# Performance work log

Hardware: AMD Instinct MI355X
Metric: run time of the kernel (lower is better)

## Reference

```python
import jax, jax.numpy as jnp
import numpy as np

B, S, DIN, D = 16, 1024, 64, 64

def setup_inputs() -> dict:
    key = jax.random.key(0)
    kx, kq, kk, kv, kaK, kaV = jax.random.split(key, 6)
    w_scale = 1.0 / np.sqrt(DIN)
    x = jax.random.normal(kx, (B, S, DIN), dtype=jnp.float32)
    Wq = jax.random.normal(kq, (DIN, D), dtype=jnp.float32) * w_scale
    Wk = jax.random.normal(kk, (DIN, D), dtype=jnp.float32) * w_scale
    Wv = jax.random.normal(kv, (DIN, D), dtype=jnp.float32) * w_scale
    # relative-position bias tables alpha_K/alpha_V: [S, S, D]
    alpha_K = jax.random.normal(kaK, (S, S, D), dtype=jnp.float32) * 0.02
    alpha_V = jax.random.normal(kaV, (S, S, D), dtype=jnp.float32) * 0.02
    return {"x": x, "Wq": Wq, "Wk": Wk, "Wv": Wv,
            "alpha_K": alpha_K, "alpha_V": alpha_V}

def reference(x, Wq, Wk, Wv, alpha_K, alpha_V):
    # Relation-aware self-attention (Shaw et al. style), vectorized form of
    # the original per-query loop:
    #   score[b,i,j] = q[b,i] . (k[b,j] + alpha_K[i,j]) / sqrt(D)
    #   z[b,i]       = sum_j softmax_j(score)[b,i,j] * (v[b,j] + alpha_V[i,j])
    d = Wq.shape[1]
    inv_sqrt_d = 1.0 / np.sqrt(d)
    q = jnp.einsum('bsf,fd->bsd', x, Wq)
    k = jnp.einsum('bsf,fd->bsd', x, Wk)
    v = jnp.einsum('bsf,fd->bsd', x, Wv)
    scores = (jnp.einsum('bid,bjd->bij', q, k)
              + jnp.einsum('bid,ijd->bij', q, alpha_K)) * inv_sqrt_d
    attn = jax.nn.softmax(scores, axis=-1)  # [B, S, S]
    z = (jnp.einsum('bij,bjd->bid', attn, v)
         + jnp.einsum('bij,ijd->bid', attn, alpha_V))
    return z, attn
```

## Files before the change

### kernel.cpp

```cpp
#include <hip/hip_runtime.h>
#include <hip/hip_fp16.h>


typedef unsigned short u16;
typedef __attribute__((ext_vector_type(8))) short bhalf8;
typedef __attribute__((ext_vector_type(4))) float fx4;

__device__ __forceinline__ u16 f2bf(float f) {
  union { float f; unsigned u; } v; v.f = f;
  unsigned r = v.u + 0x7FFFu + ((v.u >> 16) & 1u);
  return (u16)(r >> 16);
}

__device__ __forceinline__ bhalf8 pack8(float4 a, float4 b) {
  bhalf8 r;
  r[0] = (short)f2bf(a.x); r[1] = (short)f2bf(a.y); r[2] = (short)f2bf(a.z); r[3] = (short)f2bf(a.w);
  r[4] = (short)f2bf(b.x); r[5] = (short)f2bf(b.y); r[6] = (short)f2bf(b.z); r[7] = (short)f2bf(b.w);
  return r;
}

__global__ __launch_bounds__(256) void k_proj(
    const float* __restrict__ x, const float* __restrict__ Wq,
    const float* __restrict__ Wk, const float* __restrict__ Wv,
    u16* __restrict__ qbf, u16* __restrict__ kbf, float* __restrict__ vf)
{
  __shared__ float wl[3 * 4096];
  const int t = threadIdx.x;
  for (int c = t; c < 4096; c += 256) {
    wl[c] = Wq[c]; wl[4096 + c] = Wk[c]; wl[8192 + c] = Wv[c];
  }
  __syncthreads();
  const int row = blockIdx.x * 64 + (t >> 2);
  const int dbase = (t & 3) * 16;
  float xr[64];
  const float4* xp = (const float4*)(x + (size_t)row * 64);
#pragma unroll
  for (int c = 0; c < 16; ++c) {
    float4 v = xp[c];
    xr[4*c] = v.x; xr[4*c+1] = v.y; xr[4*c+2] = v.z; xr[4*c+3] = v.w;
  }
  float aq[16], ak[16], av[16];
#pragma unroll
  for (int m = 0; m < 16; ++m) { aq[m] = 0.f; ak[m] = 0.f; av[m] = 0.f; }
#pragma unroll
  for (int f = 0; f < 64; ++f) {
    const float xv = xr[f];
    const float* wq = wl + f * 64 + dbase;
#pragma unroll
    for (int m = 0; m < 16; ++m) {
      aq[m] = fmaf(xv, wq[m], aq[m]);
      ak[m] = fmaf(xv, wq[4096 + m], ak[m]);
      av[m] = fmaf(xv, wq[8192 + m], av[m]);
    }
  }
  union { u16 u[16]; uint4 q[2]; } pq, pk;
#pragma unroll
  for (int m = 0; m < 16; ++m) { pq.u[m] = f2bf(aq[m]); pk.u[m] = f2bf(ak[m]); }
  const size_t o = (size_t)row * 64 + dbase;
  *(uint4*)(qbf + o) = pq.q[0]; *(uint4*)(qbf + o + 8) = pq.q[1];
  *(uint4*)(kbf + o) = pk.q[0]; *(uint4*)(kbf + o + 8) = pk.q[1];
  float4* vo = (float4*)(vf + o);
  vo[0] = make_float4(av[0], av[1], av[2], av[3]);
  vo[1] = make_float4(av[4], av[5], av[6], av[7]);
  vo[2] = make_float4(av[8], av[9], av[10], av[11]);
  vo[3] = make_float4(av[12], av[13], av[14], av[15]);
}

__global__ __launch_bounds__(256) void k_qk(
    const u16* __restrict__ qbf, const u16* __restrict__ kbf, __half* __restrict__ qkw)
{
  const int t = threadIdx.x, l = t & 63, w = t >> 6;
  const int b = blockIdx.x & 15, it = blockIdx.x >> 4;
  const int lr = l & 15, lg = l >> 4;
  const int i0 = it * 64 + w * 16;
  const u16* qp = qbf + (size_t)(b * 1024 + i0 + lr) * 64 + lg * 8;
  bhalf8 a0 = *(const bhalf8*)(qp);
  bhalf8 a1 = *(const bhalf8*)(qp + 32);
  for (int jt = 0; jt < 64; ++jt) {
    const int j0 = jt * 16;
    const u16* kp = kbf + (size_t)(b * 1024 + j0 + lr) * 64 + lg * 8;
    bhalf8 b0 = *(const bhalf8*)(kp);
    bhalf8 b1 = *(const bhalf8*)(kp + 32);
    fx4 acc = {0.f, 0.f, 0.f, 0.f};
    acc = __builtin_amdgcn_mfma_f32_16x16x32_bf16(a0, b0, acc, 0, 0, 0);
    acc = __builtin_amdgcn_mfma_f32_16x16x32_bf16(a1, b1, acc, 0, 0, 0);
#pragma unroll
    for (int r = 0; r < 4; ++r) {
      const int i = i0 + lg * 4 + r;
      qkw[((size_t)i * 16 + b) * 1024 + j0 + lr] = __float2half(acc[r]);
    }
  }
}

#define SLD 1028
__global__ __launch_bounds__(256) void k_core(
    const float* __restrict__ aK, const float* __restrict__ aV,
    const u16* __restrict__ qbf, const __half* __restrict__ qkw,
    float* __restrict__ attn_out, float* __restrict__ za)
{
  __shared__ float sl[16 * SLD];
  __shared__ float sinv[16];
  const int i = blockIdx.x;
  const int t = threadIdx.x, l = t & 63, w = t >> 6;
  const int lr = l & 15, lg = l >> 4;

  const __half* qk = qkw + (size_t)i * 16384;
  for (int c = t; c < 16384; c += 256)
    sl[(c >> 10) * SLD + (c & 1023)] = __half2float(qk[c]);

  const u16* qp = qbf + (size_t)(lr * 1024 + i) * 64 + lg * 8;
  bhalf8 a0 = *(const bhalf8*)(qp);
  bhalf8 a1 = *(const bhalf8*)(qp + 32);
  __syncthreads();

  for (int jt = w; jt < 64; jt += 4) {
    const int j0 = jt * 16;
    const float* ap = aK + ((size_t)i * 1024 + j0 + lr) * 64 + lg * 8;
    float4 c0 = *(const float4*)(ap);
    float4 c1 = *(const float4*)(ap + 4);
    float4 c2 = *(const float4*)(ap + 32);
    float4 c3 = *(const float4*)(ap + 36);
    bhalf8 b0 = pack8(c0, c1);
    bhalf8 b1 = pack8(c2, c3);
    fx4 acc = {0.f, 0.f, 0.f, 0.f};
    acc = __builtin_amdgcn_mfma_f32_16x16x32_bf16(a0, b0, acc, 0, 0, 0);
    acc = __builtin_amdgcn_mfma_f32_16x16x32_bf16(a1, b1, acc, 0, 0, 0);
#pragma unroll
    for (int r = 0; r < 4; ++r) {
      const int bb = lg * 4 + r;
      const int j = j0 + lr;
      sl[bb * SLD + j] = (sl[bb * SLD + j] + acc[r]) * 0.125f;
    }
  }
  __syncthreads();

#pragma unroll
  for (int rr = 0; rr < 4; ++rr) {
    const int bb = w * 4 + rr;
    float e[16];
    float m = -3.0e30f;
#pragma unroll
    for (int c = 0; c < 16; ++c) { e[c] = sl[bb * SLD + c * 64 + l]; m = fmaxf(m, e[c]); }
#pragma unroll
    for (int off = 32; off; off >>= 1) m = fmaxf(m, __shfl_xor(m, off));
    float s = 0.f;
#pragma unroll
    for (int c = 0; c < 16; ++c) { e[c] = __expf(e[c] - m); s += e[c]; sl[bb * SLD + c * 64 + l] = e[c]; }
#pragma unroll
    for (int off = 32; off; off >>= 1) s += __shfl_xor(s, off);
    const float inv = 1.0f / s;
    if (l == 0) sinv[bb] = inv;
    float* ao = attn_out + ((size_t)bb * 1024 + i) * 1024;
#pragma unroll
    for (int c = 0; c < 16; ++c) ao[c * 64 + l] = e[c] * inv;
  }
  __syncthreads();

  const int d = l;
  const float* avp = aV + (size_t)i * 65536 + d;
  const float* r0 = sl + (size_t)(w + 0) * SLD;
  const float* r1 = sl + (size_t)(w + 4) * SLD;
  const float* r2 = sl + (size_t)(w + 8) * SLD;
  const float* r3 = sl + (size_t)(w + 12) * SLD;
  float z0 = 0.f, z1 = 0.f, z2 = 0.f, z3 = 0.f;
  for (int j = 0; j < 1024; j += 4) {
    float4 e0 = *(const float4*)(r0 + j);
    float4 e1 = *(const float4*)(r1 + j);
    float4 e2 = *(const float4*)(r2 + j);
    float4 e3 = *(const float4*)(r3 + j);
    float av0 = avp[(size_t)(j + 0) * 64];
    float av1 = avp[(size_t)(j + 1) * 64];
    float av2 = avp[(size_t)(j + 2) * 64];
    float av3 = avp[(size_t)(j + 3) * 64];
    z0 = fmaf(e0.x, av0, z0); z0 = fmaf(e0.y, av1, z0); z0 = fmaf(e0.z, av2, z0); z0 = fmaf(e0.w, av3, z0);
    z1 = fmaf(e1.x, av0, z1); z1 = fmaf(e1.y, av1, z1); z1 = fmaf(e1.z, av2, z1); z1 = fmaf(e1.w, av3, z1);
    z2 = fmaf(e2.x, av0, z2); z2 = fmaf(e2.y, av1, z2); z2 = fmaf(e2.z, av2, z2); z2 = fmaf(e2.w, av3, z2);
    z3 = fmaf(e3.x, av0, z3); z3 = fmaf(e3.y, av1, z3); z3 = fmaf(e3.z, av2, z3); z3 = fmaf(e3.w, av3, z3);
  }
  za[((size_t)i * 16 + w + 0) * 64 + d] = z0 * sinv[w + 0];
  za[((size_t)i * 16 + w + 4) * 64 + d] = z1 * sinv[w + 4];
  za[((size_t)i * 16 + w + 8) * 64 + d] = z2 * sinv[w + 8];
  za[((size_t)i * 16 + w + 12) * 64 + d] = z3 * sinv[w + 12];
}

__global__ __launch_bounds__(256) void k_zv(
    const float* __restrict__ attn, const float* __restrict__ vf,
    const float* __restrict__ za, float* __restrict__ zout)
{
  __shared__ __align__(16) u16 vt[64 * 40];
  const int t = threadIdx.x, l = t & 63, w = t >> 6;
  const int b = blockIdx.x & 15, it = blockIdx.x >> 4;
  const int lr = l & 15, lg = l >> 4;
  const int iw = it * 64 + w * 16;
  fx4 acc[4];
#pragma unroll
  for (int n = 0; n < 4; ++n) acc[n] = (fx4){0.f, 0.f, 0.f, 0.f};
  const int jl = t >> 3;
  const int c0 = (t & 7) * 8;
  for (int ks = 0; ks < 32; ++ks) {
    const int j0 = ks * 32;
    const float* vp = vf + (size_t)(b * 1024 + j0 + jl) * 64 + c0;
    float4 v0 = *(const float4*)(vp);
    float4 v1 = *(const float4*)(vp + 4);
    __syncthreads();
    vt[(c0 + 0) * 40 + jl] = f2bf(v0.x);
    vt[(c0 + 1) * 40 + jl] = f2bf(v0.y);
    vt[(c0 + 2) * 40 + jl] = f2bf(v0.z);
    vt[(c0 + 3) * 40 + jl] = f2bf(v0.w);
    vt[(c0 + 4) * 40 + jl] = f2bf(v1.x);
    vt[(c0 + 5) * 40 + jl] = f2bf(v1.y);
    vt[(c0 + 6) * 40 + jl] = f2bf(v1.z);
    vt[(c0 + 7) * 40 + jl] = f2bf(v1.w);
    __syncthreads();
    const float* apr = attn + (size_t)(b * 1024 + iw + lr) * 1024 + j0 + lg * 8;
    float4 t0 = *(const float4*)(apr);
    float4 t1 = *(const float4*)(apr + 4);
    bhalf8 af = pack8(t0, t1);
#pragma unroll
    for (int n = 0; n < 4; ++n) {
      bhalf8 bf = *(const bhalf8*)(vt + (n * 16 + lr) * 40 + lg * 8);
      acc[n] = __builtin_amdgcn_mfma_f32_16x16x32_bf16(af, bf, acc[n], 0, 0, 0);
    }
  }
#pragma unroll
  for (int n = 0; n < 4; ++n) {
#pragma unroll
    for (int r = 0; r < 4; ++r) {
      const int i = iw + lg * 4 + r;
      const int dd = n * 16 + lr;
      zout[((size_t)b * 1024 + i) * 64 + dd] = acc[n][r] + za[((size_t)i * 16 + b) * 64 + dd];
    }
  }
}

extern "C" void kernel_launch(void* const* d_in, const int* in_sizes, int n_in,
                              void* d_out, int out_size, void* d_ws, size_t ws_size,
                              hipStream_t stream)
{
  const float* x  = (const float*)d_in[0];
  const float* Wq = (const float*)d_in[1];
  const float* Wk = (const float*)d_in[2];
  const float* Wv = (const float*)d_in[3];
  const float* aK = (const float*)d_in[4];
  const float* aV = (const float*)d_in[5];
  float* zout = (float*)d_out;
  float* attn_out = zout + (size_t)16 * 1024 * 64;

  char* ws = (char*)d_ws;
  u16*    qbf = (u16*)(ws);
  u16*    kbf = (u16*)(ws + (size_t)2  * 1024 * 1024);
  float*  vf  = (float*)(ws + (size_t)4  * 1024 * 1024);
  float*  za  = (float*)(ws + (size_t)8  * 1024 * 1024);
  __half* qkw = (__half*)(ws + (size_t)12 * 1024 * 1024);

  hipLaunchKernelGGL(k_proj, dim3(256),  dim3(256), 0, stream, x, Wq, Wk, Wv, qbf, kbf, vf);
  hipLaunchKernelGGL(k_qk,   dim3(256),  dim3(256), 0, stream, qbf, kbf, qkw);
  hipLaunchKernelGGL(k_core, dim3(1024), dim3(256), 0, stream, aK, aV, qbf, qkw, attn_out, za);
  hipLaunchKernelGGL(k_zv,   dim3(256),  dim3(256), 0, stream, attn_out, vf, za, zout);
}
```

Before: 240.7 us.

## Split k_core over two key halves with online softmax to halve LDS

k_core now processes the 1024 keys in two halves of 512, so the shared score buffer shrinks by half and launch bounds request four blocks per CU for higher occupancy. Softmax becomes a two-pass online form: the first half's unnormalised exponentials are written out and rescaled at the end with a correction factor. The alpha_V reduction is also reorganised so each wave covers a key slice for all 16 batches, with a cross-wave sum through shared memory. The hand-written bf16 rounding is replaced by the library __float2bfloat16, and half-precision scores are loaded vectorised. The cost is extra global read-modify-write of attention rows, more barriers, and 16 accumulators per thread.

```diff
diff --git a/kernel.cpp b/kernel.cpp
--- a/kernel.cpp
+++ b/kernel.cpp
@@ -1,21 +1,21 @@
 #include <hip/hip_runtime.h>
 #include <hip/hip_fp16.h>
+#include <hip/hip_bf16.h>
 
 
 typedef unsigned short u16;
 typedef __attribute__((ext_vector_type(8))) short bhalf8;
 typedef __attribute__((ext_vector_type(4))) float fx4;
 
-__device__ __forceinline__ u16 f2bf(float f) {
-  union { float f; unsigned u; } v; v.f = f;
-  unsigned r = v.u + 0x7FFFu + ((v.u >> 16) & 1u);
-  return (u16)(r >> 16);
+__device__ __forceinline__ short b16(float f) {
+  __hip_bfloat16 h = __float2bfloat16(f);
+  return *reinterpret_cast<short*>(&h);
 }
 
 __device__ __forceinline__ bhalf8 pack8(float4 a, float4 b) {
   bhalf8 r;
-  r[0] = (short)f2bf(a.x); r[1] = (short)f2bf(a.y); r[2] = (short)f2bf(a.z); r[3] = (short)f2bf(a.w);
-  r[4] = (short)f2bf(b.x); r[5] = (short)f2bf(b.y); r[6] = (short)f2bf(b.z); r[7] = (short)f2bf(b.w);
+  r[0] = b16(a.x); r[1] = b16(a.y); r[2] = b16(a.z); r[3] = b16(a.w);
+  r[4] = b16(b.x); r[5] = b16(b.y); r[6] = b16(b.z); r[7] = b16(b.w);
   return r;
 }
 
@@ -55,7 +55,7 @@
   }
   union { u16 u[16]; uint4 q[2]; } pq, pk;
 #pragma unroll
-  for (int m = 0; m < 16; ++m) { pq.u[m] = f2bf(aq[m]); pk.u[m] = f2bf(ak[m]); }
+  for (int m = 0; m < 16; ++m) { pq.u[m] = (u16)b16(aq[m]); pk.u[m] = (u16)b16(ak[m]); }
   const size_t o = (size_t)row * 64 + dbase;
   *(uint4*)(qbf + o) = pq.q[0]; *(uint4*)(qbf + o + 8) = pq.q[1];
   *(uint4*)(kbf + o) = pk.q[0]; *(uint4*)(kbf + o + 8) = pk.q[1];
@@ -92,95 +92,151 @@
   }
 }
 
-#define SLD 1028
-__global__ __launch_bounds__(256) void k_core(
+#define SLD2 516
+__global__ __launch_bounds__(256, 4) void k_core(
     const float* __restrict__ aK, const float* __restrict__ aV,
     const u16* __restrict__ qbf, const __half* __restrict__ qkw,
     float* __restrict__ attn_out, float* __restrict__ za)
 {
-  __shared__ float sl[16 * SLD];
-  __shared__ float sinv[16];
+  __shared__ float sl[16 * SLD2];
+  __shared__ float stats[64];
   const int i = blockIdx.x;
   const int t = threadIdx.x, l = t & 63, w = t >> 6;
   const int lr = l & 15, lg = l >> 4;
 
-  const __half* qk = qkw + (size_t)i * 16384;
-  for (int c = t; c < 16384; c += 256)
-    sl[(c >> 10) * SLD + (c & 1023)] = __half2float(qk[c]);
-
   const u16* qp = qbf + (size_t)(lr * 1024 + i) * 64 + lg * 8;
   bhalf8 a0 = *(const bhalf8*)(qp);
   bhalf8 a1 = *(const bhalf8*)(qp + 32);
+
+  float zc[16];
+#pragma unroll
+  for (int b = 0; b < 16; ++b) zc[b] = 0.f;
+
+  for (int h = 0; h < 2; ++h) {
+    const __half* qk = qkw + (size_t)i * 16384 + h * 512;
+    for (int c = t; c < 1024; c += 256) {
+      const int b = c >> 6;
+      const int j8 = (c & 63) * 8;
+      const __half2* hp = (const __half2*)(qk + (size_t)b * 1024 + j8);
+      float2 f0 = __half22float2(hp[0]);
+      float2 f1 = __half22float2(hp[1]);
+      float2 f2 = __half22float2(hp[2]);
+      float2 f3 = __half22float2(hp[3]);
+      float* dst = sl + b * SLD2 + j8;
+      *(float4*)(dst)     = make_float4(f0.x, f0.y, f1.x, f1.y);
+      *(float4*)(dst + 4) = make_float4(f2.x, f2.y, f3.x, f3.y);
+    }
+    __syncthreads();
+
+    for (int tt = 0; tt < 8; ++tt) {
+      const int j0 = (w + tt * 4) * 16;
+      const float* ap = aK + ((size_t)i * 1024 + h * 512 + j0 + lr) * 64 + lg * 8;
+      float4 c0 = *(const float4*)(ap);
+      float4 c1 = *(const float4*)(ap + 4);
+      float4 c2 = *(const float4*)(ap + 32);
+      float4 c3 = *(const float4*)(ap + 36);
+      fx4 acc = {0.f, 0.f, 0.f, 0.f};
+      acc = __builtin_amdgcn_mfma_f32_16x16x32_bf16(a0, pack8(c0, c1), acc, 0, 0, 0);
+      acc = __builtin_amdgcn_mfma_f32_16x16x32_bf16(a1, pack8(c2, c3), acc, 0, 0, 0);
+#pragma unroll
+      for (int r = 0; r < 4; ++r)
+        sl[(lg * 4 + r) * SLD2 + j0 + lr] += acc[r];
+    }
+    __syncthreads();
+
+    if (h == 0) {
+#pragma unroll
+      for (int rr = 0; rr < 4; ++rr) {
+        const int row = w * 4 + rr;
+        float* rp = sl + row * SLD2;
+        float v8[8]; float mx = -3.0e30f;
+#pragma unroll
+        for (int c = 0; c < 8; ++c) { v8[c] = rp[c * 64 + l]; mx = fmaxf(mx, v8[c]); }
+#pragma unroll
+        for (int off = 32; off; off >>= 1) mx = fmaxf(mx, __shfl_xor(mx, off));
+        float sum = 0.f;
+        float* ao = attn_out + ((size_t)row * 1024 + i) * 1024;
+#pragma unroll
+        for (int c = 0; c < 8; ++c) {
+          float e = __expf((v8[c] - mx) * 0.125f);
+          sum += e; rp[c * 64 + l] = e;
+          ao[c * 64 + l] = e;
+        }
+#pragma unroll
+        for (int off = 32; off; off >>= 1) sum += __shfl_xor(sum, off);
+        if (l == 0) { stats[row] = mx; stats[16 + row] = sum; }
+      }
+    } else {
+#pragma unroll
+      for (int rr = 0; rr < 4; ++rr) {
+        const int row = w * 4 + rr;
+        float* rp = sl + row * SLD2;
+        float v8[8]; float mx = -3.0e30f;
+#pragma unroll
+        for (int c = 0; c < 8; ++c) { v8[c] = rp[c * 64 + l]; mx = fmaxf(mx, v8[c]); }
+#pragma unroll
+        for (int off = 32; off; off >>= 1) mx = fmaxf(mx, __shfl_xor(mx, off));
+        const float m1 = stats[row];
+        const float m  = fmaxf(m1, mx);
+        const float corr = __expf((m1 - m) * 0.125f);
+        float e8[8]; float sum = 0.f;
+#pragma unroll
+        for (int c = 0; c < 8; ++c) {
+          e8[c] = __expf((v8[c] - m) * 0.125f);
+          sum += e8[c]; rp[c * 64 + l] = e8[c];
+        }
+#pragma unroll
+        for (int off = 32; off; off >>= 1) sum += __shfl_xor(sum, off);
+        const float inv = 1.0f / (stats[16 + row] * corr + sum);
+        float* ao = attn_out + ((size_t)row * 1024 + i) * 1024 + 512;
+#pragma unroll
+        for (int c = 0; c < 8; ++c) ao[c * 64 + l] = e8[c] * inv;
+        if (l == 0) { stats[32 + row] = corr; stats[48 + row] = inv; }
+      }
+    }
+    __syncthreads();
+
+    if (h == 1) {
+#pragma unroll
+      for (int b = 0; b < 16; ++b) zc[b] *= stats[32 + b];
+    }
+    const float* avp = aV + ((size_t)i * 1024 + h * 512 + w * 128) * 64 + l;
+    for (int jg = 0; jg < 32; ++jg) {
+      const int jl = w * 128 + jg * 4;
+      float a0v = avp[(size_t)(jg * 4 + 0) * 64];
+      float a1v = avp[(size_t)(jg * 4 + 1) * 64];
+      float a2v = avp[(size_t)(jg * 4 + 2) * 64];
+      float a3v = avp[(size_t)(jg * 4 + 3) * 64];
+#pragma unroll
+      for (int b = 0; b < 16; ++b) {
+        float4 e4 = *(const float4*)(sl + b * SLD2 + jl);
+        zc[b] = fmaf(e4.x, a0v, zc[b]);
+        zc[b] = fmaf(e4.y, a1v, zc[b]);
+        zc[b] = fmaf(e4.z, a2v, zc[b]);
+        zc[b] = fmaf(e4.w, a3v, zc[b]);
+      }
+    }
+    __syncthreads();
+  }
+
+#pragma unroll
+  for (int b = 0; b < 16; ++b) sl[(w * 16 + b) * 64 + l] = zc[b];
   __syncthreads();
-
-  for (int jt = w; jt < 64; jt += 4) {
-    const int j0 = jt * 16;
-    const float* ap = aK + ((size_t)i * 1024 + j0 + lr) * 64 + lg * 8;
-    float4 c0 = *(const float4*)(ap);
-    float4 c1 = *(const float4*)(ap + 4);
-    float4 c2 = *(const float4*)(ap + 32);
-    float4 c3 = *(const float4*)(ap + 36);
-    bhalf8 b0 = pack8(c0, c1);
-    bhalf8 b1 = pack8(c2, c3);
-    fx4 acc = {0.f, 0.f, 0.f, 0.f};
-    acc = __builtin_amdgcn_mfma_f32_16x16x32_bf16(a0, b0, acc, 0, 0, 0);
-    acc = __builtin_amdgcn_mfma_f32_16x16x32_bf16(a1, b1, acc, 0, 0, 0);
-#pragma unroll
-    for (int r = 0; r < 4; ++r) {
-      const int bb = lg * 4 + r;
-      const int j = j0 + lr;
-      sl[bb * SLD + j] = (sl[bb * SLD + j] + acc[r]) * 0.125f;
-    }
-  }
-  __syncthreads();
+  for (int o = t; o < 1024; o += 256) {
+    const int b = o >> 6, d = o & 63;
+    float s = sl[b * 64 + d] + sl[(16 + b) * 64 + d]
+            + sl[(32 + b) * 64 + d] + sl[(48 + b) * 64 + d];
+    za[((size_t)i * 16 + b) * 64 + d] = s * stats[48 + b];
+  }
 
 #pragma unroll
   for (int rr = 0; rr < 4; ++rr) {
-    const int bb = w * 4 + rr;
-    float e[16];
-    float m = -3.0e30f;
-#pragma unroll
-    for (int c = 0; c < 16; ++c) { e[c] = sl[bb * SLD + c * 64 + l]; m = fmaxf(m, e[c]); }
-#pragma unroll
-    for (int off = 32; off; off >>= 1) m = fmaxf(m, __shfl_xor(m, off));
-    float s = 0.f;
-#pragma unroll
-    for (int c = 0; c < 16; ++c) { e[c] = __expf(e[c] - m); s += e[c]; sl[bb * SLD + c * 64 + l] = e[c]; }
-#pragma unroll
-    for (int off = 32; off; off >>= 1) s += __shfl_xor(s, off);
-    const float inv = 1.0f / s;
-    if (l == 0) sinv[bb] = inv;
-    float* ao = attn_out + ((size_t)bb * 1024 + i) * 1024;
-#pragma unroll
-    for (int c = 0; c < 16; ++c) ao[c * 64 + l] = e[c] * inv;
-  }
-  __syncthreads();
-
-  const int d = l;
-  const float* avp = aV + (size_t)i * 65536 + d;
-  const float* r0 = sl + (size_t)(w + 0) * SLD;
-  const float* r1 = sl + (size_t)(w + 4) * SLD;
-  const float* r2 = sl + (size_t)(w + 8) * SLD;
-  const float* r3 = sl + (size_t)(w + 12) * SLD;
-  float z0 = 0.f, z1 = 0.f, z2 = 0.f, z3 = 0.f;
-  for (int j = 0; j < 1024; j += 4) {
-    float4 e0 = *(const float4*)(r0 + j);
-    float4 e1 = *(const float4*)(r1 + j);
-    float4 e2 = *(const float4*)(r2 + j);
-    float4 e3 = *(const float4*)(r3 + j);
-    float av0 = avp[(size_t)(j + 0) * 64];
-    float av1 = avp[(size_t)(j + 1) * 64];
-    float av2 = avp[(size_t)(j + 2) * 64];
-    float av3 = avp[(size_t)(j + 3) * 64];
-    z0 = fmaf(e0.x, av0, z0); z0 = fmaf(e0.y, av1, z0); z0 = fmaf(e0.z, av2, z0); z0 = fmaf(e0.w, av3, z0);
-    z1 = fmaf(e1.x, av0, z1); z1 = fmaf(e1.y, av1, z1); z1 = fmaf(e1.z, av2, z1); z1 = fmaf(e1.w, av3, z1);
-    z2 = fmaf(e2.x, av0, z2); z2 = fmaf(e2.y, av1, z2); z2 = fmaf(e2.z, av2, z2); z2 = fmaf(e2.w, av3, z2);
-    z3 = fmaf(e3.x, av0, z3); z3 = fmaf(e3.y, av1, z3); z3 = fmaf(e3.z, av2, z3); z3 = fmaf(e3.w, av3, z3);
-  }
-  za[((size_t)i * 16 + w + 0) * 64 + d] = z0 * sinv[w + 0];
-  za[((size_t)i * 16 + w + 4) * 64 + d] = z1 * sinv[w + 4];
-  za[((size_t)i * 16 + w + 8) * 64 + d] = z2 * sinv[w + 8];
-  za[((size_t)i * 16 + w + 12) * 64 + d] = z3 * sinv[w + 12];
+    const int row = w * 4 + rr;
+    const float f = stats[32 + row] * stats[48 + row];
+    float* ao = attn_out + ((size_t)row * 1024 + i) * 1024;
+#pragma unroll
+    for (int c = 0; c < 8; ++c) ao[c * 64 + l] *= f;
+  }
 }
 
 __global__ __launch_bounds__(256) void k_zv(
@@ -203,14 +259,14 @@
     float4 v0 = *(const float4*)(vp);
     float4 v1 = *(const float4*)(vp + 4);
     __syncthreads();
-    vt[(c0 + 0) * 40 + jl] = f2bf(v0.x);
-    vt[(c0 + 1) * 40 + jl] = f2bf(v0.y);
-    vt[(c0 + 2) * 40 + jl] = f2bf(v0.z);
-    vt[(c0 + 3) * 40 + jl] = f2bf(v0.w);
-    vt[(c0 + 4) * 40 + jl] = f2bf(v1.x);
-    vt[(c0 + 5) * 40 + jl] = f2bf(v1.y);
-    vt[(c0 + 6) * 40 + jl] = f2bf(v1.z);
-    vt[(c0 + 7) * 40 + jl] = f2bf(v1.w);
+    vt[(c0 + 0) * 40 + jl] = (u16)b16(v0.x);
+    vt[(c0 + 1) * 40 + jl] = (u16)b16(v0.y);
+    vt[(c0 + 2) * 40 + jl] = (u16)b16(v0.z);
+    vt[(c0 + 3) * 40 + jl] = (u16)b16(v0.w);
+    vt[(c0 + 4) * 40 + jl] = (u16)b16(v1.x);
+    vt[(c0 + 5) * 40 + jl] = (u16)b16(v1.y);
+    vt[(c0 + 6) * 40 + jl] = (u16)b16(v1.z);
+    vt[(c0 + 7) * 40 + jl] = (u16)b16(v1.w);
     __syncthreads();
     const float* apr = attn + (size_t)(b * 1024 + iw + lr) * 1024 + j0 + lg * 8;
     float4 t0 = *(const float4*)(apr);
```

Result: faster. 230.0 us (-4.5%).
